# Kernel tuning notes

Hardware: AMD Instinct MI355X
Metric: run time of the kernel (lower is better)

## Reference

```python
import jax, jax.numpy as jnp
import numpy as np

SIZE = 300          # per-element hidden size (each stack item stores concat[h, c] of 2*SIZE)
TS = 64             # tracker LSTM size
B = 512             # batch
N = 128             # tokens per example
T = 2 * N - 1       # shift/reduce transitions
TRANSITION_WEIGHT = 1.0


def setup_inputs() -> dict:
    key = jax.random.key(0)
    ks = jax.random.split(key, 12)

    def he(k, shape, fan_in):
        return jax.random.normal(k, shape, jnp.float32) * np.float32(np.sqrt(2.0 / fan_in))

    inp = {
        "tokens": jax.random.normal(ks[0], (B, N, 2 * SIZE), jnp.float32),
        "Wb": he(ks[1], (SIZE, 4 * TS), SIZE),
        "Ws1": he(ks[2], (SIZE, 4 * TS), SIZE),
        "Ws2": he(ks[3], (SIZE, 4 * TS), SIZE),
        "W_ih": he(ks[4], (4 * TS, 4 * TS), 4 * TS),
        "W_hh": he(ks[5], (TS, 4 * TS), TS),
        "Wt": he(ks[6], (TS, 2), TS),
        "bt": jnp.zeros((2,), jnp.float32),
        "WL": he(ks[7], (SIZE, 5 * SIZE), SIZE),
        "WR": he(ks[8], (SIZE, 5 * SIZE), SIZE),
        "Wtr": he(ks[9], (TS, 5 * SIZE), TS),
        "bL": jnp.zeros((5 * SIZE,), jnp.float32),
    }
    # Valid SHIFT(0)/REDUCE(1) sequences: N shifts, N-1 reduces, stack>=2 before reduce.
    rng = np.random.default_rng(0)
    trans = np.zeros((B, T), np.int32)
    stack_cnt = np.zeros(B, np.int64)
    buf_cnt = np.full(B, N, np.int64)
    for i in range(T):
        can_shift = buf_cnt > 0
        can_reduce = stack_cnt >= 2
        t = ((rng.random(B) < 0.5) | ~can_shift) & can_reduce
        trans[:, i] = t.astype(np.int32)
        buf_cnt -= (~t).astype(np.int64)
        stack_cnt += np.where(t, -1, 1)
    inp["transitions"] = jnp.asarray(trans)
    return inp


def _forward(tokens, Wb, Ws1, Ws2, W_ih, W_hh, Wt, bt, WL, WR, Wtr, bL, transitions):
    Bn = tokens.shape[0]
    bidx = jnp.arange(Bn)
    sig = jax.nn.sigmoid

    def step(carry, trans_t):
        stack, sptr, bptr, th, tc = carry
        # top of buffer (buffers are consumed front-to-back in pop order)
        buf_top = tokens[bidx, jnp.minimum(bptr, N - 1)]                       # [B, 2*SIZE]
        s1 = jnp.where((sptr >= 1)[:, None], stack[bidx, jnp.clip(sptr - 1, 0, N - 1)], 0.0)
        s2 = jnp.where((sptr >= 2)[:, None], stack[bidx, jnp.clip(sptr - 2, 0, N - 1)], 0.0)
        bh = buf_top[:, :SIZE]
        s1h, s1c = s1[:, :SIZE], s1[:, SIZE:]
        s2h, s2c = s2[:, :SIZE], s2[:, SIZE:]
        # tracker: 3 bias-free linears summed, then bias-free LSTM cell
        x = bh @ Wb + s1h @ Ws1 + s2h @ Ws2                                    # [B, 4*TS]
        g = x @ W_ih + th @ W_hh
        gi, gf, gg, go = jnp.split(g, 4, axis=1)
        tc_new = sig(gf) * tc + sig(gi) * jnp.tanh(gg)
        th_new = sig(go) * jnp.tanh(tc_new)
        logits = th_new @ Wt + bt                                              # [B, 2]
        # TreeLSTM reduce composition (left = 2nd-from-top, right = top)
        r = s2h @ WL + bL + s1h @ WR + th_new @ Wtr                            # [B, 5*SIZE]
        ra, ri, rf1, rf2, ro = jnp.split(r, 5, axis=1)
        rc = jnp.tanh(ra) * sig(ri) + sig(rf1) * s2c + sig(rf2) * s1c
        rh = sig(ro) * jnp.tanh(rc)
        red = jnp.concatenate([rh, rc], axis=1)                                # [B, 2*SIZE]
        # apply transitions: 0 = SHIFT, 1 = REDUCE
        is_shift = trans_t == 0
        new_item = jnp.where(is_shift[:, None], buf_top, red)
        widx = jnp.where(is_shift, sptr, jnp.clip(sptr - 2, 0, N - 1))
        stack = stack.at[bidx, widx].set(new_item)
        sptr = jnp.where(is_shift, sptr + 1, sptr - 1)
        bptr = bptr + is_shift.astype(bptr.dtype)
        return (stack, sptr, bptr, th_new, tc_new), logits

    init = (jnp.zeros((Bn, N, 2 * SIZE), tokens.dtype),
            jnp.zeros((Bn,), jnp.int32),
            jnp.zeros((Bn,), jnp.int32),
            jnp.zeros((Bn, TS), tokens.dtype),
            jnp.zeros((Bn, TS), tokens.dtype))
    (stack, sptr, _, _, _), all_logits = jax.lax.scan(step, init, transitions.T)   # logits [T,B,2]
    final = stack[bidx, jnp.clip(sptr - 1, 0, N - 1)]                          # [B, 2*SIZE]
    logp = jax.nn.log_softmax(all_logits, axis=-1)
    nll = -jnp.take_along_axis(logp, transitions.T[..., None], axis=-1).mean()
    return final, nll * TRANSITION_WEIGHT


def reference(tokens, Wb, Ws1, Ws2, W_ih, W_hh, Wt, bt, WL, WR, Wtr, bL, transitions):
    return _forward(tokens, Wb, Ws1, Ws2, W_ih, W_hh, Wt, bt, WL, WR, Wtr, bL, transitions)
```

## Files before the change

kernel.cpp:

```cpp
#include <hip/hip_runtime.h>
#include <hip/hip_bf16.h>
#include <math.h>

#define SZ    300
#define TS    64
#define B_    512
#define NS    128
#define TT    255
#define G4    256
#define R5    1500

__device__ __forceinline__ float sigf(float x) { return 1.f / (1.f + expf(-x)); }

__global__ void kZero(int* __restrict__ nred)
{
    int i = threadIdx.x;
    if (i < TT) nred[i] = 0;
}

__global__ void kSched(const int* __restrict__ trans, int* __restrict__ sptrA,
                       int* __restrict__ bptrA, int* __restrict__ s1src,
                       int* __restrict__ s2src, int* __restrict__ finSrc,
                       int* __restrict__ redList, int* __restrict__ nred,
                       float* __restrict__ th, float* __restrict__ tc,
                       float* __restrict__ nll_row)
{
    int b = blockIdx.x * blockDim.x + threadIdx.x;
    if (b >= B_) return;
    int srcArr[NS];
    int sp = 0, bp = 0;
    for (int t = 0; t < TT; ++t) {
        sptrA[t * B_ + b] = sp;
        bptrA[t * B_ + b] = bp;
        s1src[t * B_ + b] = (sp >= 1) ? srcArr[sp - 1] : -1;
        s2src[t * B_ + b] = (sp >= 2) ? srcArr[sp - 2] : -1;
        int tr = trans[b * TT + t];
        if (tr) {
            int pos = atomicAdd(&nred[t], 1);
            redList[t * B_ + pos] = b;
            srcArr[sp - 2] = -1;
            sp -= 1;
        } else {
            srcArr[sp] = min(bp, NS - 1);
            sp += 1; bp += 1;
        }
    }
    sptrA[TT * B_ + b] = sp;
    finSrc[b] = srcArr[max(sp - 1, 0)];
    for (int k = 0; k < TS; ++k) {
        th[(size_t)b * TS + k] = 0.f;
        tc[(size_t)b * TS + k] = 0.f;
    }
    nll_row[b] = 0.f;
}

__global__ __launch_bounds__(512) void kStep1(
    const float* __restrict__ tokens, const float* __restrict__ Wb,
    const float* __restrict__ Ws1, const float* __restrict__ Ws2,
    const float* __restrict__ WL, const float* __restrict__ WR,
    const float* __restrict__ bL, const float* __restrict__ stack,
    float* __restrict__ xBuf, float* __restrict__ rPart,
    const int* __restrict__ sptrA, const int* __restrict__ bptrA,
    const int* __restrict__ s1src, const int* __restrict__ s2src,
    const int* __restrict__ redList, const int* __restrict__ nred, int t)
{
    __shared__ __align__(16) float sm[8 * 912];
    const int tid = threadIdx.x;
    const int bid = blockIdx.x;

    if (bid < 384) {
        const int chunk = bid % 12;
        const int slot  = bid / 12;
        const int col0  = chunk * 125;
        const int nr    = nred[t];
        for (int tile = slot; tile * 8 < nr; tile += 32) {
            const int base = tile * 8;
            const int cnt  = min(8, nr - base);
            for (int r = 0; r < cnt; ++r) {
                int b  = redList[t * B_ + base + r];
                int sp = sptrA[t * B_ + b];
                int i1 = s1src[t * B_ + b], i2 = s2src[t * B_ + b];
                const float* p1 = (i1 >= 0) ? tokens + ((size_t)b * NS + i1) * 600
                                            : stack  + ((size_t)b * NS + sp - 1) * 600;
                const float* p2 = (i2 >= 0) ? tokens + ((size_t)b * NS + i2) * 600
                                            : stack  + ((size_t)b * NS + sp - 2) * 600;
                for (int i = tid; i < SZ; i += 512) {
                    sm[r * 608 + i]       = p1[i];
                    sm[r * 608 + 304 + i] = p2[i];
                }
            }
            __syncthreads();
            const int c = tid & 127;
            const int q = tid >> 7;
            if (c < 125) {
                const int col = col0 + c;
                float a0 = bL[col], a1 = a0;
                const float* s0 = sm + (2 * q) * 608;
                const float* s1 = sm + (2 * q + 1) * 608;
                for (int k = 0; k < SZ; k += 4) {
                    float wr0 = WR[(size_t)(k + 0) * R5 + col];
                    float wr1 = WR[(size_t)(k + 1) * R5 + col];
                    float wr2 = WR[(size_t)(k + 2) * R5 + col];
                    float wr3 = WR[(size_t)(k + 3) * R5 + col];
                    float wl0 = WL[(size_t)(k + 0) * R5 + col];
                    float wl1 = WL[(size_t)(k + 1) * R5 + col];
                    float wl2 = WL[(size_t)(k + 2) * R5 + col];
                    float wl3 = WL[(size_t)(k + 3) * R5 + col];
                    float4 h10 = *(const float4*)&s0[k];
                    float4 h20 = *(const float4*)&s0[304 + k];
                    float4 h11 = *(const float4*)&s1[k];
                    float4 h21 = *(const float4*)&s1[304 + k];
                    a0 += h10.x * wr0 + h10.y * wr1 + h10.z * wr2 + h10.w * wr3
                        + h20.x * wl0 + h20.y * wl1 + h20.z * wl2 + h20.w * wl3;
                    a1 += h11.x * wr0 + h11.y * wr1 + h11.z * wr2 + h11.w * wr3
                        + h21.x * wl0 + h21.y * wl1 + h21.z * wl2 + h21.w * wl3;
                }
                int r0 = 2 * q, r1 = 2 * q + 1;
                if (r0 < cnt) {
                    int b = redList[t * B_ + base + r0];
                    rPart[(size_t)b * R5 + col] = a0;
                }
                if (r1 < cnt) {
                    int b = redList[t * B_ + base + r1];
                    rPart[(size_t)b * R5 + col] = a1;
                }
            }
            __syncthreads();
        }
    } else {
        const int idx  = bid - 384;
        const int rg   = idx >> 1;
        const int half = idx & 1;
        const int b0   = rg * 8;
        for (int r = 0; r < 8; ++r) {
            int b  = b0 + r;
            int sp = sptrA[t * B_ + b];
            int bp = bptrA[t * B_ + b];
            int i1 = s1src[t * B_ + b], i2 = s2src[t * B_ + b];
            const float* pb = tokens + ((size_t)b * NS + min(bp, NS - 1)) * 600;
            const float* p1 = (i1 >= 0) ? tokens + ((size_t)b * NS + i1) * 600
                                        : stack  + ((size_t)b * NS + max(sp - 1, 0)) * 600;
            const float* p2 = (i2 >= 0) ? tokens + ((size_t)b * NS + i2) * 600
                                        : stack  + ((size_t)b * NS + max(sp - 2, 0)) * 600;
            bool z1 = sp < 1, z2 = sp < 2;
            for (int i = tid; i < SZ; i += 512) {
                sm[r * 912 + i]       = pb[i];
                sm[r * 912 + 304 + i] = z1 ? 0.f : p1[i];
                sm[r * 912 + 608 + i] = z2 ? 0.f : p2[i];
            }
        }
        __syncthreads();
        const int j   = tid & 127;
        const int q   = tid >> 7;
        const int col = half * 128 + j;
        float a0 = 0.f, a1 = 0.f;
        const float* s0 = sm + (2 * q) * 912;
        const float* s1 = sm + (2 * q + 1) * 912;
        for (int k = 0; k < SZ; k += 4) {
            float wb0 = Wb [(size_t)(k + 0) * G4 + col];
            float wb1 = Wb [(size_t)(k + 1) * G4 + col];
            float wb2 = Wb [(size_t)(k + 2) * G4 + col];
            float wb3 = Wb [(size_t)(k + 3) * G4 + col];
            float w10 = Ws1[(size_t)(k + 0) * G4 + col];
            float w11 = Ws1[(size_t)(k + 1) * G4 + col];
            float w12 = Ws1[(size_t)(k + 2) * G4 + col];
            float w13 = Ws1[(size_t)(k + 3) * G4 + col];
            float w20 = Ws2[(size_t)(k + 0) * G4 + col];
            float w21 = Ws2[(size_t)(k + 1) * G4 + col];
            float w22 = Ws2[(size_t)(k + 2) * G4 + col];
            float w23 = Ws2[(size_t)(k + 3) * G4 + col];
            float4 vb0 = *(const float4*)&s0[k];
            float4 v10 = *(const float4*)&s0[304 + k];
            float4 v20 = *(const float4*)&s0[608 + k];
            float4 vb1 = *(const float4*)&s1[k];
            float4 v11 = *(const float4*)&s1[304 + k];
            float4 v21 = *(const float4*)&s1[608 + k];
            a0 += vb0.x * wb0 + vb0.y * wb1 + vb0.z * wb2 + vb0.w * wb3
                + v10.x * w10 + v10.y * w11 + v10.z * w12 + v10.w * w13
                + v20.x * w20 + v20.y * w21 + v20.z * w22 + v20.w * w23;
            a1 += vb1.x * wb0 + vb1.y * wb1 + vb1.z * wb2 + vb1.w * wb3
                + v11.x * w10 + v11.y * w11 + v11.z * w12 + v11.w * w13
                + v21.x * w20 + v21.y * w21 + v21.z * w22 + v21.w * w23;
        }
        xBuf[(size_t)(b0 + 2 * q) * G4 + col]     = a0;
        xBuf[(size_t)(b0 + 2 * q + 1) * G4 + col] = a1;
    }
}

__global__ __launch_bounds__(512) void kStep2(
    const float* __restrict__ W_ih, const float* __restrict__ W_hh,
    const float* __restrict__ Wt, const float* __restrict__ bt,
    const int* __restrict__ trans, const float* __restrict__ xBuf,
    float* __restrict__ th, float* __restrict__ tc,
    float* __restrict__ nll_row, int t)
{
    __shared__ __align__(16) float sX[8][G4];
    __shared__ __align__(16) float sTh[8][TS];
    __shared__ __align__(16) float sG[8][G4];
    __shared__ float sThn[8][TS];

    const int tid = threadIdx.x;
    const int b0  = blockIdx.x * 8;

    for (int i = tid; i < 8 * G4; i += 512) sX[i >> 8][i & 255] = xBuf[(size_t)b0 * G4 + i];
    for (int i = tid; i < 8 * TS; i += 512) sTh[i >> 6][i & 63] = th[(size_t)b0 * TS + i];
    __syncthreads();

    const int j = tid & 255;
    const int h = tid >> 8;
    float a[4] = {0.f, 0.f, 0.f, 0.f};
    for (int k = 0; k < G4; k += 4) {
        float w0 = W_ih[(size_t)(k + 0) * G4 + j];
        float w1 = W_ih[(size_t)(k + 1) * G4 + j];
        float w2 = W_ih[(size_t)(k + 2) * G4 + j];
        float w3 = W_ih[(size_t)(k + 3) * G4 + j];
        #pragma unroll
        for (int r = 0; r < 4; ++r) {
            float4 vx = *(const float4*)&sX[4 * h + r][k];
            a[r] += vx.x * w0 + vx.y * w1 + vx.z * w2 + vx.w * w3;
        }
    }
    for (int k = 0; k < TS; k += 4) {
        float w0 = W_hh[(size_t)(k + 0) * G4 + j];
        float w1 = W_hh[(size_t)(k + 1) * G4 + j];
        float w2 = W_hh[(size_t)(k + 2) * G4 + j];
        float w3 = W_hh[(size_t)(k + 3) * G4 + j];
        #pragma unroll
        for (int r = 0; r < 4; ++r) {
            float4 vt = *(const float4*)&sTh[4 * h + r][k];
            a[r] += vt.x * w0 + vt.y * w1 + vt.z * w2 + vt.w * w3;
        }
    }
    #pragma unroll
    for (int r = 0; r < 4; ++r) sG[4 * h + r][j] = a[r];
    __syncthreads();

    const int r = tid >> 6, k = tid & 63;
    const int b = b0 + r;
    {
        float gi = sG[r][k], gf = sG[r][TS + k], gg = sG[r][2 * TS + k], go = sG[r][3 * TS + k];
        float tcv = tc[(size_t)b * TS + k];
        float tcn = sigf(gf) * tcv + sigf(gi) * tanhf(gg);
        float thn = sigf(go) * tanhf(tcn);
        tc[(size_t)b * TS + k] = tcn;
        th[(size_t)b * TS + k] = thn;
        sThn[r][k] = thn;
    }
    {
        float v  = sThn[r][k];
        float p0 = v * Wt[2 * k + 0];
        float p1 = v * Wt[2 * k + 1];
        #pragma unroll
        for (int o = 32; o > 0; o >>= 1) {
            p0 += __shfl_xor(p0, o, 64);
            p1 += __shfl_xor(p1, o, 64);
        }
        if (k == 0) {
            float l0 = p0 + bt[0], l1 = p1 + bt[1];
            float m = fmaxf(l0, l1);
            float lse = m + logf(expf(l0 - m) + expf(l1 - m));
            int tr = trans[b * TT + t];
            nll_row[b] += lse - (tr ? l1 : l0);
        }
    }
}

__global__ __launch_bounds__(256) void kStep3(
    const float* __restrict__ tokens, const float* __restrict__ Wtr,
    const float* __restrict__ th, const float* __restrict__ rPart,
    float* __restrict__ stack, const int* __restrict__ sptrA,
    const int* __restrict__ s1src, const int* __restrict__ s2src,
    const int* __restrict__ redList, const int* __restrict__ nred, int t)
{
    __shared__ float sW[5][TS];
    const int tid = threadIdx.x;
    const int c   = blockIdx.x;
    for (int i = tid; i < 5 * TS; i += 256) {
        int g = i >> 6, k = i & 63;
        sW[g][k] = Wtr[(size_t)k * R5 + g * SZ + c];
    }
    __syncthreads();
    const int nr = nred[t];
    for (int jj = tid; jj < nr; jj += 256) {
        int b  = redList[t * B_ + jj];
        int sp = sptrA[t * B_ + b];
        const float* thr = th + (size_t)b * TS;
        float a0 = 0.f, a1 = 0.f, a2 = 0.f, a3 = 0.f, a4 = 0.f;
        for (int k = 0; k < TS; k += 4) {
            float4 tv = *(const float4*)&thr[k];
            a0 += tv.x * sW[0][k] + tv.y * sW[0][k+1] + tv.z * sW[0][k+2] + tv.w * sW[0][k+3];
            a1 += tv.x * sW[1][k] + tv.y * sW[1][k+1] + tv.z * sW[1][k+2] + tv.w * sW[1][k+3];
            a2 += tv.x * sW[2][k] + tv.y * sW[2][k+1] + tv.z * sW[2][k+2] + tv.w * sW[2][k+3];
            a3 += tv.x * sW[3][k] + tv.y * sW[3][k+1] + tv.z * sW[3][k+2] + tv.w * sW[3][k+3];
            a4 += tv.x * sW[4][k] + tv.y * sW[4][k+1] + tv.z * sW[4][k+2] + tv.w * sW[4][k+3];
        }
        size_t rb = (size_t)b * R5;
        float ra  = rPart[rb + 0 * SZ + c] + a0;
        float ri  = rPart[rb + 1 * SZ + c] + a1;
        float rf1 = rPart[rb + 2 * SZ + c] + a2;
        float rf2 = rPart[rb + 3 * SZ + c] + a3;
        float ro  = rPart[rb + 4 * SZ + c] + a4;
        int i1 = s1src[t * B_ + b], i2 = s2src[t * B_ + b];
        float s1c = (i1 >= 0) ? tokens[((size_t)b * NS + i1) * 600 + SZ + c]
                              : stack [((size_t)b * NS + sp - 1) * 600 + SZ + c];
        float s2c = (i2 >= 0) ? tokens[((size_t)b * NS + i2) * 600 + SZ + c]
                              : stack [((size_t)b * NS + sp - 2) * 600 + SZ + c];
        float rc = tanhf(ra) * sigf(ri) + sigf(rf1) * s2c + sigf(rf2) * s1c;
        float rh = sigf(ro) * tanhf(rc);
        float* dst = stack + ((size_t)b * NS + sp - 2) * 600;
        dst[c]      = rh;
        dst[SZ + c] = rc;
    }
}

__global__ void kFinal(const float* __restrict__ tokens, const float* __restrict__ stack,
                       const int* __restrict__ finSrc, const int* __restrict__ sptrA,
                       float* __restrict__ out)
{
    int b  = blockIdx.x;
    int fs = finSrc[b];
    int sp = sptrA[TT * B_ + b];
    int slot = max(sp - 1, 0);
    const float* src = (fs >= 0) ? tokens + ((size_t)b * NS + fs) * 600
                                 : stack  + ((size_t)b * NS + slot) * 600;
    for (int i = threadIdx.x; i < 600; i += blockDim.x)
        out[(size_t)b * 600 + i] = src[i];
}

__global__ void kNll(const float* __restrict__ nll_row, float* __restrict__ out)
{
    __shared__ float sbuf[512];
    int tid = threadIdx.x;
    sbuf[tid] = nll_row[tid];
    __syncthreads();
    for (int s = 256; s > 0; s >>= 1) {
        if (tid < s) sbuf[tid] += sbuf[tid + s];
        __syncthreads();
    }
    if (tid == 0) out[(size_t)B_ * 600] = sbuf[0] / (float)(TT * B_);
}

extern "C" void kernel_launch(void* const* d_in, const int* in_sizes, int n_in,
                              void* d_out, int out_size, void* d_ws, size_t ws_size,
                              hipStream_t stream)
{
    const float* tokens = (const float*)d_in[0];
    const float* Wb   = (const float*)d_in[1];
    const float* Ws1  = (const float*)d_in[2];
    const float* Ws2  = (const float*)d_in[3];
    const float* W_ih = (const float*)d_in[4];
    const float* W_hh = (const float*)d_in[5];
    const float* Wt   = (const float*)d_in[6];
    const float* bt   = (const float*)d_in[7];
    const float* WL   = (const float*)d_in[8];
    const float* WR   = (const float*)d_in[9];
    const float* Wtr  = (const float*)d_in[10];
    const float* bL   = (const float*)d_in[11];
    const int* trans  = (const int*)d_in[12];
    float* out = (float*)d_out;

    char* p = (char*)d_ws;
    float* stack  = (float*)p;  p += (size_t)B_ * NS * 600 * 4;
    float* xBuf   = (float*)p;  p += (size_t)B_ * G4 * 4;
    float* rPart  = (float*)p;  p += (size_t)B_ * R5 * 4;
    float* th     = (float*)p;  p += (size_t)B_ * TS * 4;
    float* tc     = (float*)p;  p += (size_t)B_ * TS * 4;
    float* nllrow = (float*)p;  p += (size_t)B_ * 4;
    int* sptrA    = (int*)p;    p += (size_t)(TT + 1) * B_ * 4;
    int* bptrA    = (int*)p;    p += (size_t)TT * B_ * 4;
    int* s1src    = (int*)p;    p += (size_t)TT * B_ * 4;
    int* s2src    = (int*)p;    p += (size_t)TT * B_ * 4;
    int* redList  = (int*)p;    p += (size_t)TT * B_ * 4;
    int* finSrc   = (int*)p;    p += (size_t)B_ * 4;
    int* nredA    = (int*)p;    p += 256 * 4;

    kZero<<<1, 256, 0, stream>>>(nredA);
    kSched<<<2, 256, 0, stream>>>(trans, sptrA, bptrA, s1src, s2src, finSrc,
                                  redList, nredA, th, tc, nllrow);
    for (int t = 0; t < TT; ++t) {
        kStep1<<<512, 512, 0, stream>>>(tokens, Wb, Ws1, Ws2, WL, WR, bL, stack,
                                        xBuf, rPart, sptrA, bptrA, s1src, s2src,
                                        redList, nredA, t);
        kStep2<<<64, 512, 0, stream>>>(W_ih, W_hh, Wt, bt, trans, xBuf, th, tc,
                                       nllrow, t);
        kStep3<<<300, 256, 0, stream>>>(tokens, Wtr, th, rPart, stack, sptrA,
                                        s1src, s2src, redList, nredA, t);
    }
    kFinal<<<512, 128, 0, stream>>>(tokens, stack, finSrc, sptrA, out);
    kNll<<<1, 512, 0, stream>>>(nllrow, out);
}
```

Measured before the change: 21.56 ms.

## Fuse all timesteps into one persistent kernel with per-block batch rows

Result: slower. 41.34 ms (+91.8%).

```diff
diff --git a/kernel.cpp b/kernel.cpp
--- a/kernel.cpp
+++ b/kernel.cpp
@@ -1,343 +1,282 @@
 #include <hip/hip_runtime.h>
-#include <hip/hip_bf16.h>
 #include <math.h>
 
-#define SZ    300
-#define TS    64
-#define B_    512
-#define NS    128
-#define TT    255
-#define G4    256
-#define R5    1500
-
-__device__ __forceinline__ float sigf(float x) { return 1.f / (1.f + expf(-x)); }
-
-__global__ void kZero(int* __restrict__ nred)
-{
-    int i = threadIdx.x;
-    if (i < TT) nred[i] = 0;
-}
-
-__global__ void kSched(const int* __restrict__ trans, int* __restrict__ sptrA,
-                       int* __restrict__ bptrA, int* __restrict__ s1src,
-                       int* __restrict__ s2src, int* __restrict__ finSrc,
-                       int* __restrict__ redList, int* __restrict__ nred,
-                       float* __restrict__ th, float* __restrict__ tc,
-                       float* __restrict__ nll_row)
-{
-    int b = blockIdx.x * blockDim.x + threadIdx.x;
-    if (b >= B_) return;
-    int srcArr[NS];
-    int sp = 0, bp = 0;
-    for (int t = 0; t < TT; ++t) {
-        sptrA[t * B_ + b] = sp;
-        bptrA[t * B_ + b] = bp;
-        s1src[t * B_ + b] = (sp >= 1) ? srcArr[sp - 1] : -1;
-        s2src[t * B_ + b] = (sp >= 2) ? srcArr[sp - 2] : -1;
-        int tr = trans[b * TT + t];
-        if (tr) {
-            int pos = atomicAdd(&nred[t], 1);
-            redList[t * B_ + pos] = b;
-            srcArr[sp - 2] = -1;
-            sp -= 1;
-        } else {
-            srcArr[sp] = min(bp, NS - 1);
-            sp += 1; bp += 1;
-        }
-    }
-    sptrA[TT * B_ + b] = sp;
-    finSrc[b] = srcArr[max(sp - 1, 0)];
-    for (int k = 0; k < TS; ++k) {
-        th[(size_t)b * TS + k] = 0.f;
-        tc[(size_t)b * TS + k] = 0.f;
-    }
-    nll_row[b] = 0.f;
-}
-
-__global__ __launch_bounds__(512) void kStep1(
+#define SZ 300
+#define TS 64
+#define B_ 512
+#define NS 128
+#define TT 255
+#define G4 256
+#define R5 1500
+#define RPB 4
+#define NBLK (B_/RPB)
+#define NTHR 512
+
+__device__ __forceinline__ float sigf(float x){ return 1.f/(1.f+expf(-x)); }
+
+__global__ __launch_bounds__(NTHR) void kSpinn(
     const float* __restrict__ tokens, const float* __restrict__ Wb,
     const float* __restrict__ Ws1, const float* __restrict__ Ws2,
+    const float* __restrict__ W_ih, const float* __restrict__ W_hh,
+    const float* __restrict__ Wt, const float* __restrict__ bt,
     const float* __restrict__ WL, const float* __restrict__ WR,
-    const float* __restrict__ bL, const float* __restrict__ stack,
-    float* __restrict__ xBuf, float* __restrict__ rPart,
-    const int* __restrict__ sptrA, const int* __restrict__ bptrA,
-    const int* __restrict__ s1src, const int* __restrict__ s2src,
-    const int* __restrict__ redList, const int* __restrict__ nred, int t)
+    const float* __restrict__ Wtr, const float* __restrict__ bL,
+    const int* __restrict__ trans, float* __restrict__ stack,
+    float* __restrict__ out, float* __restrict__ nllrow)
 {
-    __shared__ __align__(16) float sm[8 * 912];
+    __shared__ __align__(16) float sInp[RPB][912];
+    __shared__ __align__(16) float sX[RPB][G4];
+    __shared__ __align__(16) float sG[RPB][G4];
+    __shared__ __align__(16) float sTh[RPB][TS];
+    __shared__ __align__(16) float sTc[RPB][TS];
+    __shared__ __align__(16) float sR[RPB][R5];
+    __shared__ int srcS[RPB][NS];
+    __shared__ int sTr[RPB], sS1[RPB], sS2[RPB];
+    __shared__ int sS1sl[RPB], sS2sl[RPB], sWsl[RPB], sBpl[RPB];
+    __shared__ float sNll[RPB];
+
     const int tid = threadIdx.x;
-    const int bid = blockIdx.x;
-
-    if (bid < 384) {
-        const int chunk = bid % 12;
-        const int slot  = bid / 12;
-        const int col0  = chunk * 125;
-        const int nr    = nred[t];
-        for (int tile = slot; tile * 8 < nr; tile += 32) {
-            const int base = tile * 8;
-            const int cnt  = min(8, nr - base);
-            for (int r = 0; r < cnt; ++r) {
-                int b  = redList[t * B_ + base + r];
-                int sp = sptrA[t * B_ + b];
-                int i1 = s1src[t * B_ + b], i2 = s2src[t * B_ + b];
-                const float* p1 = (i1 >= 0) ? tokens + ((size_t)b * NS + i1) * 600
-                                            : stack  + ((size_t)b * NS + sp - 1) * 600;
-                const float* p2 = (i2 >= 0) ? tokens + ((size_t)b * NS + i2) * 600
-                                            : stack  + ((size_t)b * NS + sp - 2) * 600;
-                for (int i = tid; i < SZ; i += 512) {
-                    sm[r * 608 + i]       = p1[i];
-                    sm[r * 608 + 304 + i] = p2[i];
-                }
-            }
-            __syncthreads();
-            const int c = tid & 127;
-            const int q = tid >> 7;
-            if (c < 125) {
-                const int col = col0 + c;
-                float a0 = bL[col], a1 = a0;
-                const float* s0 = sm + (2 * q) * 608;
-                const float* s1 = sm + (2 * q + 1) * 608;
+    const int b0 = blockIdx.x * RPB;
+
+    for (int i = tid; i < RPB*TS; i += NTHR) { sTh[i>>6][i&63] = 0.f; sTc[i>>6][i&63] = 0.f; }
+    if (tid < RPB) sNll[tid] = 0.f;
+    int sp = 0, bp = 0, prevTr = 0;
+
+    for (int t = 0; t < TT; ++t) {
+        __syncthreads();
+
+        if (tid < RPB) {
+            int r = tid, b = b0 + r;
+            if (t > 0) {
+                if (prevTr) { srcS[r][sp-2] = -1; sp -= 1; }
+                else        { if (sp < NS) srcS[r][sp] = bp; sp += 1; bp += 1; }
+            }
+            int tr = trans[b*TT + t];
+            sTr[r] = tr; prevTr = tr;
+            int s1sl = min(max(sp-1,0), NS-1), s2sl = min(max(sp-2,0), NS-1);
+            sS1sl[r] = s1sl; sS2sl[r] = s2sl;
+            sS1[r] = (sp >= 1) ? srcS[r][s1sl] : -3;
+            sS2[r] = (sp >= 2) ? srcS[r][s2sl] : -3;
+            sWsl[r] = min(max(sp-2,0), NS-1);
+            sBpl[r] = min(bp, NS-1);
+        }
+        __syncthreads();
+
+        for (int idx = tid; idx < RPB*912; idx += NTHR) {
+            int r = idx / 912, pos = idx - r*912;
+            int b = b0 + r;
+            float v = 0.f;
+            if (pos < 304) {
+                int i = pos;
+                if (i < SZ) v = tokens[((size_t)b*NS + sBpl[r])*600 + i];
+            } else if (pos < 608) {
+                int i = pos - 304, c = sS1[r];
+                if (i < SZ && c != -3)
+                    v = (c >= 0) ? tokens[((size_t)b*NS + c)*600 + i]
+                                 : stack [((size_t)b*NS + sS1sl[r])*600 + i];
+            } else {
+                int i = pos - 608, c = sS2[r];
+                if (i < SZ && c != -3)
+                    v = (c >= 0) ? tokens[((size_t)b*NS + c)*600 + i]
+                                 : stack [((size_t)b*NS + sS2sl[r])*600 + i];
+            }
+            sInp[r][pos] = v;
+        }
+        __syncthreads();
+
+        {
+            const int j = tid & 255, h = tid >> 8;
+            float a0 = 0.f, a1 = 0.f;
+            const float* i0 = sInp[2*h];
+            const float* i1 = sInp[2*h+1];
+            #pragma unroll 1
+            for (int m = 0; m < 3; ++m) {
+                const float* W = (m == 0) ? Wb : ((m == 1) ? Ws1 : Ws2);
+                const int off = m * 304;
                 for (int k = 0; k < SZ; k += 4) {
-                    float wr0 = WR[(size_t)(k + 0) * R5 + col];
-                    float wr1 = WR[(size_t)(k + 1) * R5 + col];
-                    float wr2 = WR[(size_t)(k + 2) * R5 + col];
-                    float wr3 = WR[(size_t)(k + 3) * R5 + col];
-                    float wl0 = WL[(size_t)(k + 0) * R5 + col];
-                    float wl1 = WL[(size_t)(k + 1) * R5 + col];
-                    float wl2 = WL[(size_t)(k + 2) * R5 + col];
-                    float wl3 = WL[(size_t)(k + 3) * R5 + col];
-                    float4 h10 = *(const float4*)&s0[k];
-                    float4 h20 = *(const float4*)&s0[304 + k];
-                    float4 h11 = *(const float4*)&s1[k];
-                    float4 h21 = *(const float4*)&s1[304 + k];
-                    a0 += h10.x * wr0 + h10.y * wr1 + h10.z * wr2 + h10.w * wr3
-                        + h20.x * wl0 + h20.y * wl1 + h20.z * wl2 + h20.w * wl3;
-                    a1 += h11.x * wr0 + h11.y * wr1 + h11.z * wr2 + h11.w * wr3
-                        + h21.x * wl0 + h21.y * wl1 + h21.z * wl2 + h21.w * wl3;
-                }
-                int r0 = 2 * q, r1 = 2 * q + 1;
-                if (r0 < cnt) {
-                    int b = redList[t * B_ + base + r0];
-                    rPart[(size_t)b * R5 + col] = a0;
-                }
-                if (r1 < cnt) {
-                    int b = redList[t * B_ + base + r1];
-                    rPart[(size_t)b * R5 + col] = a1;
-                }
-            }
-            __syncthreads();
-        }
-    } else {
-        const int idx  = bid - 384;
-        const int rg   = idx >> 1;
-        const int half = idx & 1;
-        const int b0   = rg * 8;
-        for (int r = 0; r < 8; ++r) {
-            int b  = b0 + r;
-            int sp = sptrA[t * B_ + b];
-            int bp = bptrA[t * B_ + b];
-            int i1 = s1src[t * B_ + b], i2 = s2src[t * B_ + b];
-            const float* pb = tokens + ((size_t)b * NS + min(bp, NS - 1)) * 600;
-            const float* p1 = (i1 >= 0) ? tokens + ((size_t)b * NS + i1) * 600
-                                        : stack  + ((size_t)b * NS + max(sp - 1, 0)) * 600;
-            const float* p2 = (i2 >= 0) ? tokens + ((size_t)b * NS + i2) * 600
-                                        : stack  + ((size_t)b * NS + max(sp - 2, 0)) * 600;
-            bool z1 = sp < 1, z2 = sp < 2;
-            for (int i = tid; i < SZ; i += 512) {
-                sm[r * 912 + i]       = pb[i];
-                sm[r * 912 + 304 + i] = z1 ? 0.f : p1[i];
-                sm[r * 912 + 608 + i] = z2 ? 0.f : p2[i];
-            }
-        }
-        __syncthreads();
-        const int j   = tid & 127;
-        const int q   = tid >> 7;
-        const int col = half * 128 + j;
-        float a0 = 0.f, a1 = 0.f;
-        const float* s0 = sm + (2 * q) * 912;
-        const float* s1 = sm + (2 * q + 1) * 912;
-        for (int k = 0; k < SZ; k += 4) {
-            float wb0 = Wb [(size_t)(k + 0) * G4 + col];
-            float wb1 = Wb [(size_t)(k + 1) * G4 + col];
-            float wb2 = Wb [(size_t)(k + 2) * G4 + col];
-            float wb3 = Wb [(size_t)(k + 3) * G4 + col];
-            float w10 = Ws1[(size_t)(k + 0) * G4 + col];
-            float w11 = Ws1[(size_t)(k + 1) * G4 + col];
-            float w12 = Ws1[(size_t)(k + 2) * G4 + col];
-            float w13 = Ws1[(size_t)(k + 3) * G4 + col];
-            float w20 = Ws2[(size_t)(k + 0) * G4 + col];
-            float w21 = Ws2[(size_t)(k + 1) * G4 + col];
-            float w22 = Ws2[(size_t)(k + 2) * G4 + col];
-            float w23 = Ws2[(size_t)(k + 3) * G4 + col];
-            float4 vb0 = *(const float4*)&s0[k];
-            float4 v10 = *(const float4*)&s0[304 + k];
-            float4 v20 = *(const float4*)&s0[608 + k];
-            float4 vb1 = *(const float4*)&s1[k];
-            float4 v11 = *(const float4*)&s1[304 + k];
-            float4 v21 = *(const float4*)&s1[608 + k];
-            a0 += vb0.x * wb0 + vb0.y * wb1 + vb0.z * wb2 + vb0.w * wb3
-                + v10.x * w10 + v10.y * w11 + v10.z * w12 + v10.w * w13
-                + v20.x * w20 + v20.y * w21 + v20.z * w22 + v20.w * w23;
-            a1 += vb1.x * wb0 + vb1.y * wb1 + vb1.z * wb2 + vb1.w * wb3
-                + v11.x * w10 + v11.y * w11 + v11.z * w12 + v11.w * w13
-                + v21.x * w20 + v21.y * w21 + v21.z * w22 + v21.w * w23;
-        }
-        xBuf[(size_t)(b0 + 2 * q) * G4 + col]     = a0;
-        xBuf[(size_t)(b0 + 2 * q + 1) * G4 + col] = a1;
+                    float w0 = W[(k+0)*G4+j], w1 = W[(k+1)*G4+j];
+                    float w2 = W[(k+2)*G4+j], w3 = W[(k+3)*G4+j];
+                    float4 v0 = *(const float4*)&i0[off+k];
+                    float4 v1 = *(const float4*)&i1[off+k];
+                    a0 += v0.x*w0 + v0.y*w1 + v0.z*w2 + v0.w*w3;
+                    a1 += v1.x*w0 + v1.y*w1 + v1.z*w2 + v1.w*w3;
+                }
+            }
+            sX[2*h][j] = a0; sX[2*h+1][j] = a1;
+        }
+        __syncthreads();
+
+        {
+            const int j = tid & 255, h = tid >> 8;
+            float a0 = 0.f, a1 = 0.f;
+            const float* x0 = sX[2*h];
+            const float* x1 = sX[2*h+1];
+            for (int k = 0; k < G4; k += 4) {
+                float w0 = W_ih[(k+0)*G4+j], w1 = W_ih[(k+1)*G4+j];
+                float w2 = W_ih[(k+2)*G4+j], w3 = W_ih[(k+3)*G4+j];
+                float4 v0 = *(const float4*)&x0[k];
+                float4 v1 = *(const float4*)&x1[k];
+                a0 += v0.x*w0 + v0.y*w1 + v0.z*w2 + v0.w*w3;
+                a1 += v1.x*w0 + v1.y*w1 + v1.z*w2 + v1.w*w3;
+            }
+            const float* t0 = sTh[2*h];
+            const float* t1 = sTh[2*h+1];
+            for (int k = 0; k < TS; k += 4) {
+                float w0 = W_hh[(k+0)*G4+j], w1 = W_hh[(k+1)*G4+j];
+                float w2 = W_hh[(k+2)*G4+j], w3 = W_hh[(k+3)*G4+j];
+                float4 v0 = *(const float4*)&t0[k];
+                float4 v1 = *(const float4*)&t1[k];
+                a0 += v0.x*w0 + v0.y*w1 + v0.z*w2 + v0.w*w3;
+                a1 += v1.x*w0 + v1.y*w1 + v1.z*w2 + v1.w*w3;
+            }
+            sG[2*h][j] = a0; sG[2*h+1][j] = a1;
+        }
+        __syncthreads();
+
+        if (tid < RPB*TS) {
+            int r = tid >> 6, k = tid & 63;
+            float gi = sG[r][k], gf = sG[r][TS+k], gg = sG[r][2*TS+k], go = sG[r][3*TS+k];
+            float tcn = sigf(gf)*sTc[r][k] + sigf(gi)*tanhf(gg);
+            float thn = sigf(go)*tanhf(tcn);
+            sTc[r][k] = tcn; sTh[r][k] = thn;
+            float p0 = thn * Wt[2*k + 0];
+            float p1 = thn * Wt[2*k + 1];
+            #pragma unroll
+            for (int o = 32; o > 0; o >>= 1) {
+                p0 += __shfl_xor(p0, o, 64);
+                p1 += __shfl_xor(p1, o, 64);
+            }
+            if (k == 0) {
+                float l0 = p0 + bt[0], l1 = p1 + bt[1];
+                float m = fmaxf(l0, l1);
+                float lse = m + logf(expf(l0-m) + expf(l1-m));
+                sNll[r] += lse - (sTr[r] ? l1 : l0);
+            }
+        }
+        __syncthreads();
+
+        const int anyRed = sTr[0] | sTr[1] | sTr[2] | sTr[3];
+        if (anyRed) {
+            const bool a0 = sTr[0], a1 = sTr[1], a2 = sTr[2], a3 = sTr[3];
+            const int c0 = tid, c1 = tid + 512, c2 = tid + 1024;
+            float acc[RPB][3];
+            #pragma unroll
+            for (int r = 0; r < RPB; ++r) {
+                acc[r][0] = bL[c0];
+                acc[r][1] = bL[c1];
+                acc[r][2] = (c2 < R5) ? bL[c2] : 0.f;
+            }
+            for (int k = 0; k < SZ; k += 4) {
+                float wl[4][3], wr[4][3];
+                #pragma unroll
+                for (int kk = 0; kk < 4; ++kk) {
+                    wl[kk][0] = WL[(size_t)(k+kk)*R5 + c0];
+                    wl[kk][1] = WL[(size_t)(k+kk)*R5 + c1];
+                    wl[kk][2] = WL[(size_t)(k+kk)*R5 + c2];
+                    wr[kk][0] = WR[(size_t)(k+kk)*R5 + c0];
+                    wr[kk][1] = WR[(size_t)(k+kk)*R5 + c1];
+                    wr[kk][2] = WR[(size_t)(k+kk)*R5 + c2];
+                }
+                #pragma unroll
+                for (int r = 0; r < RPB; ++r) {
+                    bool act = (r==0) ? a0 : (r==1) ? a1 : (r==2) ? a2 : a3;
+                    if (act) {
+                        float4 h2 = *(const float4*)&sInp[r][608 + k];
+                        float4 h1 = *(const float4*)&sInp[r][304 + k];
+                        #pragma unroll
+                        for (int p = 0; p < 3; ++p) {
+                            acc[r][p] += h2.x*wl[0][p] + h2.y*wl[1][p] + h2.z*wl[2][p] + h2.w*wl[3][p]
+                                       + h1.x*wr[0][p] + h1.y*wr[1][p] + h1.z*wr[2][p] + h1.w*wr[3][p];
+                        }
+                    }
+                }
+            }
+            for (int k = 0; k < TS; k += 4) {
+                float wt[4][3];
+                #pragma unroll
+                for (int kk = 0; kk < 4; ++kk) {
+                    wt[kk][0] = Wtr[(size_t)(k+kk)*R5 + c0];
+                    wt[kk][1] = Wtr[(size_t)(k+kk)*R5 + c1];
+                    wt[kk][2] = Wtr[(size_t)(k+kk)*R5 + c2];
+                }
+                #pragma unroll
+                for (int r = 0; r < RPB; ++r) {
+                    bool act = (r==0) ? a0 : (r==1) ? a1 : (r==2) ? a2 : a3;
+                    if (act) {
+                        float4 tv = *(const float4*)&sTh[r][k];
+                        #pragma unroll
+                        for (int p = 0; p < 3; ++p)
+                            acc[r][p] += tv.x*wt[0][p] + tv.y*wt[1][p] + tv.z*wt[2][p] + tv.w*wt[3][p];
+                    }
+                }
+            }
+            #pragma unroll
+            for (int r = 0; r < RPB; ++r) {
+                bool act = (r==0) ? a0 : (r==1) ? a1 : (r==2) ? a2 : a3;
+                if (act) {
+                    sR[r][c0] = acc[r][0];
+                    sR[r][c1] = acc[r][1];
+                    if (c2 < R5) sR[r][c2] = acc[r][2];
+                }
+            }
+        }
+        __syncthreads();
+
+        if (anyRed) {
+            for (int idx = tid; idx < RPB*SZ; idx += NTHR) {
+                int r = idx / SZ, c = idx - r*SZ;
+                if (sTr[r]) {
+                    int b = b0 + r;
+                    float ra  = sR[r][c],        ri = sR[r][SZ+c], rf1 = sR[r][2*SZ+c];
+                    float rf2 = sR[r][3*SZ+c],   ro = sR[r][4*SZ+c];
+                    int cc1 = sS1[r], cc2 = sS2[r];
+                    float s1c = (cc1 >= 0) ? tokens[((size_t)b*NS + cc1)*600 + SZ + c]
+                                           : stack [((size_t)b*NS + sS1sl[r])*600 + SZ + c];
+                    float s2c = (cc2 >= 0) ? tokens[((size_t)b*NS + cc2)*600 + SZ + c]
+                                           : stack [((size_t)b*NS + sS2sl[r])*600 + SZ + c];
+                    float rc = tanhf(ra)*sigf(ri) + sigf(rf1)*s2c + sigf(rf2)*s1c;
+                    float rh = sigf(ro)*tanhf(rc);
+                    float* dst = stack + ((size_t)b*NS + sWsl[r])*600;
+                    dst[c]      = rh;
+                    dst[SZ + c] = rc;
+                }
+            }
+        }
+    }
+
+    __syncthreads();
+    if (tid < RPB) {
+        int r = tid;
+        if (prevTr) { srcS[r][sp-2] = -1; sp -= 1; }
+        else        { if (sp < NS) srcS[r][sp] = bp; sp += 1; bp += 1; }
+        int fsl = min(max(sp-1,0), NS-1);
+        sS1sl[r] = fsl;
+        sS1[r] = (sp >= 1) ? srcS[r][fsl] : -3;
+        nllrow[b0 + r] = sNll[r];
+    }
+    __syncthreads();
+    for (int idx = tid; idx < RPB*600; idx += NTHR) {
+        int r = idx / 600, i = idx - r*600;
+        int b = b0 + r;
+        int c = sS1[r];
+        float v = 0.f;
+        if (c >= 0)       v = tokens[((size_t)b*NS + c)*600 + i];
+        else if (c == -1) v = stack [((size_t)b*NS + sS1sl[r])*600 + i];
+        out[(size_t)b*600 + i] = v;
     }
 }
 
-__global__ __launch_bounds__(512) void kStep2(
-    const float* __restrict__ W_ih, const float* __restrict__ W_hh,
-    const float* __restrict__ Wt, const float* __restrict__ bt,
-    const int* __restrict__ trans, const float* __restrict__ xBuf,
-    float* __restrict__ th, float* __restrict__ tc,
-    float* __restrict__ nll_row, int t)
+__global__ void kNll(const float* __restrict__ nllrow, float* __restrict__ out)
 {
-    __shared__ __align__(16) float sX[8][G4];
-    __shared__ __align__(16) float sTh[8][TS];
-    __shared__ __align__(16) float sG[8][G4];
-    __shared__ float sThn[8][TS];
-
-    const int tid = threadIdx.x;
-    const int b0  = blockIdx.x * 8;
-
-    for (int i = tid; i < 8 * G4; i += 512) sX[i >> 8][i & 255] = xBuf[(size_t)b0 * G4 + i];
-    for (int i = tid; i < 8 * TS; i += 512) sTh[i >> 6][i & 63] = th[(size_t)b0 * TS + i];
-    __syncthreads();
-
-    const int j = tid & 255;
-    const int h = tid >> 8;
-    float a[4] = {0.f, 0.f, 0.f, 0.f};
-    for (int k = 0; k < G4; k += 4) {
-        float w0 = W_ih[(size_t)(k + 0) * G4 + j];
-        float w1 = W_ih[(size_t)(k + 1) * G4 + j];
-        float w2 = W_ih[(size_t)(k + 2) * G4 + j];
-        float w3 = W_ih[(size_t)(k + 3) * G4 + j];
-        #pragma unroll
-        for (int r = 0; r < 4; ++r) {
-            float4 vx = *(const float4*)&sX[4 * h + r][k];
-            a[r] += vx.x * w0 + vx.y * w1 + vx.z * w2 + vx.w * w3;
-        }
-    }
-    for (int k = 0; k < TS; k += 4) {
-        float w0 = W_hh[(size_t)(k + 0) * G4 + j];
-        float w1 = W_hh[(size_t)(k + 1) * G4 + j];
-        float w2 = W_hh[(size_t)(k + 2) * G4 + j];
-        float w3 = W_hh[(size_t)(k + 3) * G4 + j];
-        #pragma unroll
-        for (int r = 0; r < 4; ++r) {
-            float4 vt = *(const float4*)&sTh[4 * h + r][k];
-            a[r] += vt.x * w0 + vt.y * w1 + vt.z * w2 + vt.w * w3;
-        }
-    }
-    #pragma unroll
-    for (int r = 0; r < 4; ++r) sG[4 * h + r][j] = a[r];
-    __syncthreads();
-
-    const int r = tid >> 6, k = tid & 63;
-    const int b = b0 + r;
-    {
-        float gi = sG[r][k], gf = sG[r][TS + k], gg = sG[r][2 * TS + k], go = sG[r][3 * TS + k];
-        float tcv = tc[(size_t)b * TS + k];
-        float tcn = sigf(gf) * tcv + sigf(gi) * tanhf(gg);
-        float thn = sigf(go) * tanhf(tcn);
-        tc[(size_t)b * TS + k] = tcn;
-        th[(size_t)b * TS + k] = thn;
-        sThn[r][k] = thn;
-    }
-    {
-        float v  = sThn[r][k];
-        float p0 = v * Wt[2 * k + 0];
-        float p1 = v * Wt[2 * k + 1];
-        #pragma unroll
-        for (int o = 32; o > 0; o >>= 1) {
-            p0 += __shfl_xor(p0, o, 64);
-            p1 += __shfl_xor(p1, o, 64);
-        }
-        if (k == 0) {
-            float l0 = p0 + bt[0], l1 = p1 + bt[1];
-            float m = fmaxf(l0, l1);
-            float lse = m + logf(expf(l0 - m) + expf(l1 - m));
-            int tr = trans[b * TT + t];
-            nll_row[b] += lse - (tr ? l1 : l0);
-        }
-    }
-}
-
-__global__ __launch_bounds__(256) void kStep3(
-    const float* __restrict__ tokens, const float* __restrict__ Wtr,
-    const float* __restrict__ th, const float* __restrict__ rPart,
-    float* __restrict__ stack, const int* __restrict__ sptrA,
-    const int* __restrict__ s1src, const int* __restrict__ s2src,
-    const int* __restrict__ redList, const int* __restrict__ nred, int t)
-{
-    __shared__ float sW[5][TS];
-    const int tid = threadIdx.x;
-    const int c   = blockIdx.x;
-    for (int i = tid; i < 5 * TS; i += 256) {
-        int g = i >> 6, k = i & 63;
-        sW[g][k] = Wtr[(size_t)k * R5 + g * SZ + c];
-    }
-    __syncthreads();
-    const int nr = nred[t];
-    for (int jj = tid; jj < nr; jj += 256) {
-        int b  = redList[t * B_ + jj];
-        int sp = sptrA[t * B_ + b];
-        const float* thr = th + (size_t)b * TS;
-        float a0 = 0.f, a1 = 0.f, a2 = 0.f, a3 = 0.f, a4 = 0.f;
-        for (int k = 0; k < TS; k += 4) {
-            float4 tv = *(const float4*)&thr[k];
-            a0 += tv.x * sW[0][k] + tv.y * sW[0][k+1] + tv.z * sW[0][k+2] + tv.w * sW[0][k+3];
-            a1 += tv.x * sW[1][k] + tv.y * sW[1][k+1] + tv.z * sW[1][k+2] + tv.w * sW[1][k+3];
-            a2 += tv.x * sW[2][k] + tv.y * sW[2][k+1] + tv.z * sW[2][k+2] + tv.w * sW[2][k+3];
-            a3 += tv.x * sW[3][k] + tv.y * sW[3][k+1] + tv.z * sW[3][k+2] + tv.w * sW[3][k+3];
-            a4 += tv.x * sW[4][k] + tv.y * sW[4][k+1] + tv.z * sW[4][k+2] + tv.w * sW[4][k+3];
-        }
-        size_t rb = (size_t)b * R5;
-        float ra  = rPart[rb + 0 * SZ + c] + a0;
-        float ri  = rPart[rb + 1 * SZ + c] + a1;
-        float rf1 = rPart[rb + 2 * SZ + c] + a2;
-        float rf2 = rPart[rb + 3 * SZ + c] + a3;
-        float ro  = rPart[rb + 4 * SZ + c] + a4;
-        int i1 = s1src[t * B_ + b], i2 = s2src[t * B_ + b];
-        float s1c = (i1 >= 0) ? tokens[((size_t)b * NS + i1) * 600 + SZ + c]
-                              : stack [((size_t)b * NS + sp - 1) * 600 + SZ + c];
-        float s2c = (i2 >= 0) ? tokens[((size_t)b * NS + i2) * 600 + SZ + c]
-                              : stack [((size_t)b * NS + sp - 2) * 600 + SZ + c];
-        float rc = tanhf(ra) * sigf(ri) + sigf(rf1) * s2c + sigf(rf2) * s1c;
-        float rh = sigf(ro) * tanhf(rc);
-        float* dst = stack + ((size_t)b * NS + sp - 2) * 600;
-        dst[c]      = rh;
-        dst[SZ + c] = rc;
-    }
-}
-
-__global__ void kFinal(const float* __restrict__ tokens, const float* __restrict__ stack,
-                       const int* __restrict__ finSrc, const int* __restrict__ sptrA,
-                       float* __restrict__ out)
-{
-    int b  = blockIdx.x;
-    int fs = finSrc[b];
-    int sp = sptrA[TT * B_ + b];
-    int slot = max(sp - 1, 0);
-    const float* src = (fs >= 0) ? tokens + ((size_t)b * NS + fs) * 600
-                                 : stack  + ((size_t)b * NS + slot) * 600;
-    for (int i = threadIdx.x; i < 600; i += blockDim.x)
-        out[(size_t)b * 600 + i] = src[i];
-}
-
-__global__ void kNll(const float* __restrict__ nll_row, float* __restrict__ out)
-{
-    __shared__ float sbuf[512];
+    __shared__ float sb[512];
     int tid = threadIdx.x;
-    sbuf[tid] = nll_row[tid];
+    sb[tid] = nllrow[tid];
     __syncthreads();
     for (int s = 256; s > 0; s >>= 1) {
-        if (tid < s) sbuf[tid] += sbuf[tid + s];
+        if (tid < s) sb[tid] += sb[tid + s];
         __syncthreads();
     }
-    if (tid == 0) out[(size_t)B_ * 600] = sbuf[0] / (float)(TT * B_);
+    if (tid == 0) out[(size_t)B_*600] = sb[0] / (float)(TT * B_);
 }
 
 extern "C" void kernel_launch(void* const* d_in, const int* in_sizes, int n_in,
@@ -361,31 +300,9 @@
 
     char* p = (char*)d_ws;
     float* stack  = (float*)p;  p += (size_t)B_ * NS * 600 * 4;
-    float* xBuf   = (float*)p;  p += (size_t)B_ * G4 * 4;
-    float* rPart  = (float*)p;  p += (size_t)B_ * R5 * 4;
-    float* th     = (float*)p;  p += (size_t)B_ * TS * 4;
-    float* tc     = (float*)p;  p += (size_t)B_ * TS * 4;
     float* nllrow = (float*)p;  p += (size_t)B_ * 4;
-    int* sptrA    = (int*)p;    p += (size_t)(TT + 1) * B_ * 4;
-    int* bptrA    = (int*)p;    p += (size_t)TT * B_ * 4;
-    int* s1src    = (int*)p;    p += (size_t)TT * B_ * 4;
-    int* s2src    = (int*)p;    p += (size_t)TT * B_ * 4;
-    int* redList  = (int*)p;    p += (size_t)TT * B_ * 4;
-    int* finSrc   = (int*)p;    p += (size_t)B_ * 4;
-    int* nredA    = (int*)p;    p += 256 * 4;
-
-    kZero<<<1, 256, 0, stream>>>(nredA);
-    kSched<<<2, 256, 0, stream>>>(trans, sptrA, bptrA, s1src, s2src, finSrc,
-                                  redList, nredA, th, tc, nllrow);
-    for (int t = 0; t < TT; ++t) {
-        kStep1<<<512, 512, 0, stream>>>(tokens, Wb, Ws1, Ws2, WL, WR, bL, stack,
-                                        xBuf, rPart, sptrA, bptrA, s1src, s2src,
-                                        redList, nredA, t);
-        kStep2<<<64, 512, 0, stream>>>(W_ih, W_hh, Wt, bt, trans, xBuf, th, tc,
-                                       nllrow, t);
-        kStep3<<<300, 256, 0, stream>>>(tokens, Wtr, th, rPart, stack, sptrA,
-                                        s1src, s2src, redList, nredA, t);
-    }
-    kFinal<<<512, 128, 0, stream>>>(tokens, stack, finSrc, sptrA, out);
+
+    kSpinn<<<NBLK, NTHR, 0, stream>>>(tokens, Wb, Ws1, Ws2, W_ih, W_hh, Wt, bt,
+                                      WL, WR, Wtr, bL, trans, stack, out, nllrow);
     kNll<<<1, 512, 0, stream>>>(nllrow, out);
 }
```
